# Kernel tuning notes

Hardware: AMD Instinct MI355X
Metric: run time of the kernel (lower is better)

## Reference

```python
import jax, jax.numpy as jnp
import numpy as np

DIM_Q = 1024
DIM_KV = 768
N_HEADS = 4


def setup_inputs() -> dict:
    key = jax.random.key(0)
    ks = jax.random.split(key, 7)
    b, lq, lkv = 4, 2048, 2048
    q = jax.random.normal(ks[0], (b, lq, DIM_Q), dtype=jnp.float32)
    kv = jax.random.normal(ks[1], (b, lkv, DIM_KV), dtype=jnp.float32)
    s_q = 1.0 / np.sqrt(DIM_Q)
    s_kv = 1.0 / np.sqrt(DIM_KV)
    Wq = jax.random.normal(ks[2], (DIM_Q, DIM_Q), dtype=jnp.float32) * s_q
    Wk = jax.random.normal(ks[3], (DIM_Q, DIM_KV), dtype=jnp.float32) * s_kv
    Wv = jax.random.normal(ks[4], (DIM_Q, DIM_KV), dtype=jnp.float32) * s_kv
    Wo = jax.random.normal(ks[5], (DIM_Q, DIM_Q), dtype=jnp.float32) * s_q
    bo = jax.random.normal(ks[6], (DIM_Q,), dtype=jnp.float32) * 0.01
    return {"q": q, "kv": kv, "Wq": Wq, "Wk": Wk, "Wv": Wv, "Wo": Wo, "bo": bo}


def _split_heads(x):
    # [b, l, d] -> [b, h, l, d/h]
    b, l, d = x.shape
    return x.reshape(b, l, N_HEADS, d // N_HEADS).transpose(0, 2, 1, 3)


def reference(q, kv, Wq, Wk, Wv, Wo, bo):
    qp = q @ Wq.T               # [b, lq, dim_q]
    kp = kv @ Wk.T              # [b, lkv, dim_q]
    vp = kv @ Wv.T              # [b, lkv, dim_q]
    qh, kh, vh = _split_heads(qp), _split_heads(kp), _split_heads(vp)
    scale = (DIM_Q // N_HEADS) ** (-0.5)
    scores = jnp.einsum('bhqd,bhkd->bhqk', qh, kh) * scale
    attn = jax.nn.softmax(scores, axis=-1)
    ctx = jnp.einsum('bhqk,bhkd->bhqd', attn, vh)  # [b, h, lq, hd]
    b, h, lq, hd = ctx.shape
    ctx = ctx.transpose(0, 2, 1, 3).reshape(b, lq, h * hd)
    return ctx @ Wo.T + bo
```

## Files before the change

### kernel.cpp

```cpp
#include <hip/hip_runtime.h>

#define DIMQ 1024
#define NH 4
#define HD 256
#define BSZ 4
#define LQ 2048
#define LKV 2048
#define KVN 2048

typedef __attribute__((ext_vector_type(8))) short bf16x8;
typedef __attribute__((ext_vector_type(4))) float f32x4;

__device__ inline unsigned short f32_to_bf16(float f) {
  union { float f; unsigned u; } v; v.f = f;
  unsigned u = v.u;
  return (unsigned short)((u + 0x7fffu + ((u >> 16) & 1u)) >> 16);
}

__device__ inline uint4 ld8cvt(const float* p, float scale) {
  const float4 a = *(const float4*)p;
  const float4 b = *(const float4*)(p + 4);
  union { unsigned short s[8]; uint4 v; } r;
  r.s[0] = f32_to_bf16(a.x * scale); r.s[1] = f32_to_bf16(a.y * scale);
  r.s[2] = f32_to_bf16(a.z * scale); r.s[3] = f32_to_bf16(a.w * scale);
  r.s[4] = f32_to_bf16(b.x * scale); r.s[5] = f32_to_bf16(b.y * scale);
  r.s[6] = f32_to_bf16(b.z * scale); r.s[7] = f32_to_bf16(b.w * scale);
  return r.v;
}

__device__ __forceinline__ void gl2lds16(const void* gptr, void* lptr) {
  __builtin_amdgcn_global_load_lds(
      (const __attribute__((address_space(1))) void*)gptr,
      (__attribute__((address_space(3))) void*)lptr, 16, 0, 0);
}

__global__ __launch_bounds__(256)
void cvt6(const float* s0, const float* s1, const float* s2, const float* s3,
          const float* s4, const float* s5,
          unsigned short* d0, unsigned short* d1, unsigned short* d2,
          unsigned short* d3, unsigned short* d4, unsigned short* d5,
          long n0, long n1, long n2, long n3, long n4, long n5,
          float c0, float c1, float c2, float c3, float c4, float c5) {
  const float* s; unsigned short* d; long n; float c;
  switch (blockIdx.y) {
    case 0: s = s0; d = d0; n = n0; c = c0; break;
    case 1: s = s1; d = d1; n = n1; c = c1; break;
    case 2: s = s2; d = d2; n = n2; c = c2; break;
    case 3: s = s3; d = d3; n = n3; c = c3; break;
    case 4: s = s4; d = d4; n = n4; c = c4; break;
    default: s = s5; d = d5; n = n5; c = c5; break;
  }
  long i = ((long)blockIdx.x * 256 + threadIdx.x) * 8;
  if (i < n) *(uint4*)(d + i) = ld8cvt(s + i, c);
}

__global__ __launch_bounds__(256)
void transpose_k(const unsigned short* __restrict__ vp,
                 unsigned short* __restrict__ vpT,
                 int src_stride, int src_off) {
  __shared__ unsigned short T[64][64];
  const int l0g = blockIdx.x * 64;
  const int b = l0g / LKV, l0 = l0g % LKV;
  const int n0 = blockIdx.y * 64;
  const int tid = threadIdx.x;
  const int r = tid >> 3, c = tid & 7;
#pragma unroll
  for (int p = 0; p < 2; ++p) {
    int row = p * 32 + r;
    *(uint4*)&T[row][(c ^ ((row >> 3) & 7)) * 8] =
        *(const uint4*)(vp + (size_t)(l0g + row) * src_stride + src_off + n0 + c * 8);
  }
  __syncthreads();
#pragma unroll
  for (int p = 0; p < 2; ++p) {
    int n = p * 32 + r;
    union { unsigned short s[8]; uint4 v; } t;
#pragma unroll
    for (int j = 0; j < 8; ++j) {
      int row = c * 8 + j;
      t.s[j] = T[row][(((n >> 3) ^ ((row >> 3) & 7)) << 3) | (n & 7)];
    }
    *(uint4*)(vpT + ((size_t)b * DIMQ + n0 + n) * LKV + l0 + c * 8) = t.v;
  }
}

template<typename TOUT, bool HAS_BIAS>
__global__ __launch_bounds__(256)
void gemm_bt(const unsigned short* __restrict__ A,
             const unsigned short* __restrict__ Bm,
             const float* __restrict__ bias,
             TOUT* __restrict__ C,
             int M, int N, int K) {
  __shared__ alignas(16) unsigned short As[128 * 64];
  __shared__ alignas(16) unsigned short Bs[128 * 64];
  const int tid = threadIdx.x;
  const int lane = tid & 63;
  const int wave = tid >> 6;
  const int wr = (wave >> 1) * 64, wc = (wave & 1) * 64;
  const int l15 = lane & 15, quad = lane >> 4;
  const int srow = lane >> 3, scol = lane & 7;
  const int m0 = blockIdx.x * 128;
  const int n0 = blockIdx.y * 128;

  f32x4 acc[4][4] = {};
  for (int k0 = 0; k0 < K; k0 += 64) {
    __syncthreads();
#pragma unroll
    for (int i = 0; i < 4; ++i) {
      int c = wave * 4 + i;
      gl2lds16(A + (size_t)(m0 + c * 8 + srow) * K + k0 + scol * 8, As + c * 512);
      gl2lds16(Bm + (size_t)(n0 + c * 8 + srow) * K + k0 + scol * 8, Bs + c * 512);
    }
    __syncthreads();
#pragma unroll
    for (int kh = 0; kh < 2; ++kh) {
      bf16x8 af[4], bfr[4];
#pragma unroll
      for (int i = 0; i < 4; ++i)
        af[i] = *(const bf16x8*)(As + (wr + i * 16 + l15) * 64 + kh * 32 + quad * 8);
#pragma unroll
      for (int j = 0; j < 4; ++j)
        bfr[j] = *(const bf16x8*)(Bs + (wc + j * 16 + l15) * 64 + kh * 32 + quad * 8);
#pragma unroll
      for (int i = 0; i < 4; ++i)
#pragma unroll
        for (int j = 0; j < 4; ++j)
          acc[i][j] = __builtin_amdgcn_mfma_f32_16x16x32_bf16(af[i], bfr[j], acc[i][j], 0, 0, 0);
    }
  }

#pragma unroll
  for (int j = 0; j < 4; ++j) {
    int n = n0 + wc + j * 16 + l15;
    float bv = 0.f;
    if (HAS_BIAS) bv = bias[n];
#pragma unroll
    for (int i = 0; i < 4; ++i) {
      int mb = m0 + wr + i * 16 + quad * 4;
#pragma unroll
      for (int r = 0; r < 4; ++r) {
        float v = acc[i][j][r] + bv;
        if constexpr (sizeof(TOUT) == 2)
          C[(size_t)(mb + r) * N + n] = f32_to_bf16(v);
        else
          C[(size_t)(mb + r) * N + n] = v;
      }
    }
  }
}

__global__ __launch_bounds__(256, 2)
void attn(const unsigned short* __restrict__ qp,
          const unsigned short* __restrict__ kpv,
          const unsigned short* __restrict__ vpT,
          unsigned short* __restrict__ ctx) {
  __shared__ alignas(16) unsigned short Ks[64 * 256];
  __shared__ alignas(16) unsigned short Vt[256 * 64];
  __shared__ alignas(16) unsigned short Ps[64 * 64];
  __shared__ float Ls[64][2];
  const int tid = threadIdx.x, lane = tid & 63, wave = tid >> 6;
  const int l15 = lane & 15, quad = lane >> 4;
  const int qh = wave >> 1;
  const int kvh = wave & 1;
  const int b = blockIdx.z, h = blockIdx.y;
  const int q0 = blockIdx.x * 64;
  const size_t base = (size_t)b * LQ * DIMQ + h * HD;

  bf16x8 qf[2][8];
#pragma unroll
  for (int im = 0; im < 2; ++im) {
    const unsigned short* qrow =
        qp + base + (size_t)(q0 + qh * 32 + im * 16 + l15) * DIMQ;
#pragma unroll
    for (int s = 0; s < 8; ++s)
      qf[im][s] = *(const bf16x8*)(qrow + s * 32 + quad * 8);
  }

  f32x4 oacc[2][8] = {};
  float lrow[2][4] = {};

  const unsigned short* kb = kpv + (size_t)b * LKV * KVN + h * HD;
  const unsigned short* vtb = vpT + ((size_t)b * DIMQ + h * HD) * LKV;

  const int krow_l = lane >> 5;
  const int kcol_l = lane & 31;
  const int vrow_l = lane >> 3;
  const int vcol_l = lane & 7;

#pragma unroll
  for (int i = 0; i < 8; ++i) {
    int c = i * 4 + wave;
    int row = 2 * c + krow_l;
    int lr = (row & 32) + ((row & 15) << 1) + ((row >> 4) & 1);
    gl2lds16(kb + (size_t)lr * KVN + ((kcol_l ^ (row & 7)) << 3), Ks + c * 512);
  }
  __syncthreads();

  for (int kv0 = 0; kv0 < LKV; kv0 += 64) {
#pragma unroll
    for (int i = 0; i < 8; ++i) {
      int c = i * 4 + wave;
      int row = 8 * c + vrow_l;
      gl2lds16(vtb + (size_t)row * LKV + kv0 + ((vcol_l ^ (row & 7)) << 3),
               Vt + c * 512);
    }

    f32x4 sacc[2][2] = {};
    const int r0 = kvh * 32 + l15, r1 = r0 + 16;
    __builtin_amdgcn_s_setprio(1);
#pragma unroll
    for (int s = 0; s < 8; ++s) {
      bf16x8 kf0 = *(const bf16x8*)(Ks + r0 * 256 + (((s * 4 + quad) ^ (r0 & 7)) << 3));
      bf16x8 kf1 = *(const bf16x8*)(Ks + r1 * 256 + (((s * 4 + quad) ^ (r1 & 7)) << 3));
      sacc[0][0] = __builtin_amdgcn_mfma_f32_16x16x32_bf16(qf[0][s], kf0, sacc[0][0], 0, 0, 0);
      sacc[0][1] = __builtin_amdgcn_mfma_f32_16x16x32_bf16(qf[0][s], kf1, sacc[0][1], 0, 0, 0);
      sacc[1][0] = __builtin_amdgcn_mfma_f32_16x16x32_bf16(qf[1][s], kf0, sacc[1][0], 0, 0, 0);
      sacc[1][1] = __builtin_amdgcn_mfma_f32_16x16x32_bf16(qf[1][s], kf1, sacc[1][1], 0, 0, 0);
    }
    __builtin_amdgcn_s_setprio(0);

    const int dw = kvh * 16 + l15;
    const int t16 = dw >> 2, sub = dw & 3;
#pragma unroll
    for (int im = 0; im < 2; ++im)
#pragma unroll
      for (int i = 0; i < 4; ++i) {
        int row = qh * 32 + im * 16 + quad * 4 + i;
        float p0 = exp2f(sacc[im][0][i]);
        float p1 = exp2f(sacc[im][1][i]);
        unsigned pw = (unsigned)f32_to_bf16(p0) | ((unsigned)f32_to_bf16(p1) << 16);
        *(unsigned*)(Ps + row * 64 + (((t16 ^ (row & 7)) << 3) | (sub * 2))) = pw;
        lrow[im][i] += p0 + p1;
      }
    __syncthreads();

    if (kv0 + 64 < LKV) {
#pragma unroll
      for (int i = 0; i < 8; ++i) {
        int c = i * 4 + wave;
        int row = 2 * c + krow_l;
        int lr = (row & 32) + ((row & 15) << 1) + ((row >> 4) & 1);
        gl2lds16(kb + (size_t)(kv0 + 64 + lr) * KVN + ((kcol_l ^ (row & 7)) << 3),
                 Ks + c * 512);
      }
    }

    const int pr0 = qh * 32 + l15, pr1 = pr0 + 16;
    __builtin_amdgcn_s_setprio(1);
#pragma unroll
    for (int u = 0; u < 2; ++u) {
      bf16x8 pf0 = *(const bf16x8*)(Ps + pr0 * 64 + (((u * 4 + quad) ^ (pr0 & 7)) << 3));
      bf16x8 pf1 = *(const bf16x8*)(Ps + pr1 * 64 + (((u * 4 + quad) ^ (pr1 & 7)) << 3));
#pragma unroll
      for (int jn = 0; jn < 8; ++jn) {
        int vr = kvh * 128 + jn * 16 + l15;
        bf16x8 vf = *(const bf16x8*)(Vt + vr * 64 + (((u * 4 + quad) ^ (vr & 7)) << 3));
        oacc[0][jn] = __builtin_amdgcn_mfma_f32_16x16x32_bf16(pf0, vf, oacc[0][jn], 0, 0, 0);
        oacc[1][jn] = __builtin_amdgcn_mfma_f32_16x16x32_bf16(pf1, vf, oacc[1][jn], 0, 0, 0);
      }
    }
    __builtin_amdgcn_s_setprio(0);
    __syncthreads();
  }

#pragma unroll
  for (int im = 0; im < 2; ++im)
#pragma unroll
    for (int i = 0; i < 4; ++i) {
      float l = lrow[im][i];
      l += __shfl_xor(l, 1);
      l += __shfl_xor(l, 2);
      l += __shfl_xor(l, 4);
      l += __shfl_xor(l, 8);
      if (l15 == 0) Ls[qh * 32 + im * 16 + quad * 4 + i][kvh] = l;
    }
  __syncthreads();

  unsigned short* cb = ctx + base;
#pragma unroll
  for (int im = 0; im < 2; ++im)
#pragma unroll
    for (int r = 0; r < 4; ++r) {
      int row = qh * 32 + im * 16 + quad * 4 + r;
      float inv = 1.0f / (Ls[row][0] + Ls[row][1]);
#pragma unroll
      for (int jn = 0; jn < 8; ++jn) {
        int col = kvh * 128 + jn * 16 + l15;
        cb[(size_t)(q0 + row) * DIMQ + col] = f32_to_bf16(oacc[im][jn][r] * inv);
      }
    }
}

extern "C" void kernel_launch(void* const* d_in, const int* in_sizes, int n_in,
                              void* d_out, int out_size, void* d_ws, size_t ws_size,
                              hipStream_t stream) {
  const float* q  = (const float*)d_in[0];
  const float* kv = (const float*)d_in[1];
  const float* Wq = (const float*)d_in[2];
  const float* Wk = (const float*)d_in[3];
  const float* Wv = (const float*)d_in[4];
  const float* Wo = (const float*)d_in[5];
  const float* bo = (const float*)d_in[6];
  float* out = (float*)d_out;

  const long NQ = (long)BSZ * LQ * DIMQ;
  const long NKV = (long)BSZ * LKV * 768;
  const long NWQ = (long)DIMQ * DIMQ;
  const long NWK = (long)DIMQ * 768;

  unsigned short* q_bf = (unsigned short*)d_out;
  unsigned short* kpv  = (unsigned short*)d_out;
  unsigned short* kv_bf = (unsigned short*)d_ws;
  unsigned short* ctx   = kv_bf;
  unsigned short* Wq_bf = kv_bf + NQ;
  unsigned short* Wk_bf = Wq_bf + NWQ;
  unsigned short* Wv_bf = Wk_bf + NWK;
  unsigned short* Wo_bf = Wv_bf + NWK;
  unsigned short* qp    = Wo_bf + NWQ;
  unsigned short* vpT   = qp + NQ;

  dim3 blk(256);
  const int M = BSZ * LQ;

  cvt6<<<dim3(4096, 6), blk, 0, stream>>>(
      kv, Wq, Wk, Wv, Wo, q,
      kv_bf, Wq_bf, Wk_bf, Wv_bf, Wo_bf, q_bf,
      NKV, NWQ, NWK, NWK, NWQ, NQ,
      1.0f, 0.0625f * 1.44269504088896f, 1.0f, 1.0f, 1.0f, 1.0f);
  gemm_bt<unsigned short, false><<<dim3(M/128, DIMQ/128), blk, 0, stream>>>(q_bf, Wq_bf, nullptr, qp, M, DIMQ, 1024);
  gemm_bt<unsigned short, false><<<dim3(M/128, KVN/128), blk, 0, stream>>>(kv_bf, Wk_bf, nullptr, kpv, M, KVN, 768);
  transpose_k<<<dim3(M/64, DIMQ/64), blk, 0, stream>>>(kpv, vpT, KVN, 1024);
  attn<<<dim3(LQ/64, NH, BSZ), blk, 0, stream>>>(qp, kpv, vpT, ctx);
  gemm_bt<float, true><<<dim3(M/128, DIMQ/128), blk, 0, stream>>>(ctx, Wo_bf, bo, out, M, DIMQ, 1024);
}
```

Baseline: 307.5 us.

## Retile PV matmul per wave over output columns and remap blocks for L2 locality

The P·V stage now gives each wave all 64 query rows and a 64-column slice of the head dimension, replacing the old 32 rows by 128 columns split. Each wave loads 4 P fragments and 4 V fragments per k-step instead of 2 and 8, which cuts LDS reads per MFMA. The grid also becomes 1D with a swizzled mapping that spreads consecutive blocks across (b, h) groups so that blocks running together share K/V in cache. The final normalisation still reads Ls, which holds both kvh partial sums, so the result stays correct.

Measured after the change: 302.5 us. No clear change (-1.6%).

```diff
diff --git a/kernel.cpp b/kernel.cpp
--- a/kernel.cpp
+++ b/kernel.cpp
@@ -162,8 +162,10 @@
   const int l15 = lane & 15, quad = lane >> 4;
   const int qh = wave >> 1;
   const int kvh = wave & 1;
-  const int b = blockIdx.z, h = blockIdx.y;
-  const int q0 = blockIdx.x * 64;
+  const int lin = blockIdx.x;
+  const int work = ((lin & 7) << 6) + (lin >> 3);
+  const int b = work >> 7, h = (work >> 5) & 3;
+  const int q0 = (work & 31) * 64;
   const size_t base = (size_t)b * LQ * DIMQ + h * HD;
 
   bf16x8 qf[2][8];
@@ -176,7 +178,7 @@
       qf[im][s] = *(const bf16x8*)(qrow + s * 32 + quad * 8);
   }
 
-  f32x4 oacc[2][8] = {};
+  f32x4 oacc[4][4] = {};
   float lrow[2][4] = {};
 
   const unsigned short* kb = kpv + (size_t)b * LKV * KVN + h * HD;
@@ -245,19 +247,25 @@
       }
     }
 
-    const int pr0 = qh * 32 + l15, pr1 = pr0 + 16;
     __builtin_amdgcn_s_setprio(1);
 #pragma unroll
     for (int u = 0; u < 2; ++u) {
-      bf16x8 pf0 = *(const bf16x8*)(Ps + pr0 * 64 + (((u * 4 + quad) ^ (pr0 & 7)) << 3));
-      bf16x8 pf1 = *(const bf16x8*)(Ps + pr1 * 64 + (((u * 4 + quad) ^ (pr1 & 7)) << 3));
-#pragma unroll
-      for (int jn = 0; jn < 8; ++jn) {
-        int vr = kvh * 128 + jn * 16 + l15;
-        bf16x8 vf = *(const bf16x8*)(Vt + vr * 64 + (((u * 4 + quad) ^ (vr & 7)) << 3));
-        oacc[0][jn] = __builtin_amdgcn_mfma_f32_16x16x32_bf16(pf0, vf, oacc[0][jn], 0, 0, 0);
-        oacc[1][jn] = __builtin_amdgcn_mfma_f32_16x16x32_bf16(pf1, vf, oacc[1][jn], 0, 0, 0);
-      }
+      bf16x8 pf[4], vf[4];
+#pragma unroll
+      for (int mt = 0; mt < 4; ++mt) {
+        int pr = mt * 16 + l15;
+        pf[mt] = *(const bf16x8*)(Ps + pr * 64 + (((u * 4 + quad) ^ (pr & 7)) << 3));
+      }
+#pragma unroll
+      for (int nt = 0; nt < 4; ++nt) {
+        int vr = wave * 64 + nt * 16 + l15;
+        vf[nt] = *(const bf16x8*)(Vt + vr * 64 + (((u * 4 + quad) ^ (vr & 7)) << 3));
+      }
+#pragma unroll
+      for (int mt = 0; mt < 4; ++mt)
+#pragma unroll
+        for (int nt = 0; nt < 4; ++nt)
+          oacc[mt][nt] = __builtin_amdgcn_mfma_f32_16x16x32_bf16(pf[mt], vf[nt], oacc[mt][nt], 0, 0, 0);
     }
     __builtin_amdgcn_s_setprio(0);
     __syncthreads();
@@ -278,15 +286,15 @@
 
   unsigned short* cb = ctx + base;
 #pragma unroll
-  for (int im = 0; im < 2; ++im)
+  for (int mt = 0; mt < 4; ++mt)
 #pragma unroll
     for (int r = 0; r < 4; ++r) {
-      int row = qh * 32 + im * 16 + quad * 4 + r;
+      int row = mt * 16 + quad * 4 + r;
       float inv = 1.0f / (Ls[row][0] + Ls[row][1]);
 #pragma unroll
-      for (int jn = 0; jn < 8; ++jn) {
-        int col = kvh * 128 + jn * 16 + l15;
-        cb[(size_t)(q0 + row) * DIMQ + col] = f32_to_bf16(oacc[im][jn][r] * inv);
+      for (int nt = 0; nt < 4; ++nt) {
+        int col = wave * 64 + nt * 16 + l15;
+        cb[(size_t)(q0 + row) * DIMQ + col] = f32_to_bf16(oacc[mt][nt][r] * inv);
       }
     }
 }
@@ -330,6 +338,6 @@
   gemm_bt<unsigned short, false><<<dim3(M/128, DIMQ/128), blk, 0, stream>>>(q_bf, Wq_bf, nullptr, qp, M, DIMQ, 1024);
   gemm_bt<unsigned short, false><<<dim3(M/128, KVN/128), blk, 0, stream>>>(kv_bf, Wk_bf, nullptr, kpv, M, KVN, 768);
   transpose_k<<<dim3(M/64, DIMQ/64), blk, 0, stream>>>(kpv, vpT, KVN, 1024);
-  attn<<<dim3(LQ/64, NH, BSZ), blk, 0, stream>>>(qp, kpv, vpT, ctx);
+  attn<<<dim3(512), blk, 0, stream>>>(qp, kpv, vpT, ctx);
   gemm_bt<float, true><<<dim3(M/128, DIMQ/128), blk, 0, stream>>>(ctx, Wo_bf, bo, out, M, DIMQ, 1024);
 }
```
